# Optimization experiments

Hardware: AMD Instinct MI355X
Metric: run time of the kernel (lower is better)

The kernel has to match this reference:

```python
import jax, jax.numpy as jnp
import numpy as np

B, T, N_X, N_U, N_Y, H = 2048, 2048, 4, 2, 1, 64
MIN_X = jnp.array([0.0, 0.0, 0.0, -jnp.inf], dtype=jnp.float32)
MAX_X = jnp.array([10.0, 10.0, 10.0, jnp.inf], dtype=jnp.float32)
MIN_Y = jnp.array([0.0], dtype=jnp.float32)
MAX_Y = jnp.array([10.0], dtype=jnp.float32)


def setup_inputs() -> dict:
    key = jax.random.key(0)
    ks = jax.random.split(key, 6)
    return {
        "x_0": jax.random.uniform(ks[0], (B, N_X), dtype=jnp.float32) * 5.0,
        "u": jax.random.normal(ks[1], (B, T, N_U), dtype=jnp.float32),
        "theta_f": jnp.array([0.1925, 0.2429, 0.1697, 0.0444, 0.1642], dtype=jnp.float32),
        "theta_h": jnp.zeros((1,), dtype=jnp.float32),
        "tau_u": jnp.ones((1,), dtype=jnp.float32),
        "tau_y": jnp.ones((1,), dtype=jnp.float32),
        "W1": jax.random.normal(ks[2], (N_X + N_U + 5, H), dtype=jnp.float32) / np.sqrt(N_X + N_U + 5),
        "b1": jnp.zeros((H,), dtype=jnp.float32),
        "W2": jax.random.normal(ks[3], (H, N_X), dtype=jnp.float32) * 0.05,
        "Wh": jax.random.normal(ks[4], (N_X, N_Y), dtype=jnp.float32),
    }


def reference(x_0, u, theta_f, theta_h, tau_u, tau_y, W1, b1, W2, Wh):
    Bc = x_0.shape[0]
    tf = jnp.broadcast_to(theta_f[None, :], (Bc, theta_f.shape[0]))
    scale = tau_u[0] / tau_y[0]

    def f(x, ut):
        feat = jnp.concatenate([x, ut, tf], axis=-1)  # (B, n_x+n_u+5)
        return jnp.tanh(feat @ W1 + b1) @ W2 * scale  # (B, n_x)

    def h(x):
        return x @ Wh + theta_h  # (B, n_y)

    y0 = h(x_0)  # unclamped initial output, as in the torch loop

    def step(carry, ut):
        x_step, y_step = carry
        dx = f(x_step, ut)
        x_raw = x_step + dx
        y_new = jnp.clip(h(x_raw), MIN_Y, MAX_Y)  # y computed from pre-clamp state
        x_new = jnp.clip(x_raw, MIN_X, MAX_X)
        return (x_new, y_new), (x_step, y_step)

    u_t = jnp.moveaxis(u, 1, 0)  # (T, B, n_u)
    _, (xs, ys) = jax.lax.scan(step, (x_0, y0), u_t)
    x = jnp.moveaxis(xs, 0, 1)  # (B, T, n_x)
    y = jnp.moveaxis(ys, 0, 1)  # (B, T, n_y)
    return (x, y)
```

## Files before the change

kernel.cpp:

```cpp
#include <hip/hip_runtime.h>

#define B_SZ 2048
#define T_SZ 2048

using f32x16 = float __attribute__((ext_vector_type(16)));
using f32x2  = float __attribute__((ext_vector_type(2)));

template<int CTRL>
__device__ __forceinline__ float dppf(float v) {
  int r = __builtin_amdgcn_update_dpp(0, __builtin_bit_cast(int, v), CTRL, 0xf, 0xf, true);
  return __builtin_bit_cast(float, r);
}

__device__ __forceinline__ f32x2 pkfma(f32x2 a, f32x2 b, f32x2 c) {
  return __builtin_elementwise_fma(a, b, c);
}

__global__ __launch_bounds__(256) void sss_kernel(
    const float* __restrict__ x0p, const float* __restrict__ up,
    const float* __restrict__ tfp, const float* __restrict__ thp,
    const float* __restrict__ tup, const float* __restrict__ typ,
    const float* __restrict__ W1p, const float* __restrict__ b1p,
    const float* __restrict__ W2p, const float* __restrict__ Whp,
    float* __restrict__ outp)
{
  const int lane = threadIdx.x & 63;
  const int wv   = __builtin_amdgcn_readfirstlane((int)(threadIdx.x >> 6));
  const int grp  = lane >> 4;
  const int sl   = lane & 15;
  const int k    = lane & 3;
  const int b    = blockIdx.x * 16 + wv * 4 + grp;

  const float K = 2.8853900817779268f;
  f32x2 w1_01[6], w1_23[6];
#pragma unroll
  for (int r = 0; r < 6; ++r) {
    w1_01[r] = f32x2{W1p[r * 64 + sl]      * K, W1p[r * 64 + sl + 16] * K};
    w1_23[r] = f32x2{W1p[r * 64 + sl + 32] * K, W1p[r * 64 + sl + 48] * K};
  }
  float ccs[4];
#pragma unroll
  for (int i = 0; i < 4; ++i) {
    const int u = sl + 16 * i;
    float t = b1p[u];
#pragma unroll
    for (int q = 0; q < 5; ++q) t = fmaf(tfp[q], W1p[(6 + q) * 64 + u], t);
    ccs[i] = t * K;
  }
  const f32x2 cc01 = f32x2{ccs[0], ccs[1]};
  const f32x2 cc23 = f32x2{ccs[2], ccs[3]};

  const float scale = tup[0] / typ[0];
  f32x2 wAB[4], wCD[4];
#pragma unroll
  for (int i = 0; i < 4; ++i) {
    const float4 w2r = ((const float4*)W2p)[sl + 16 * i];
    float col[4] = {w2r.x * scale, w2r.y * scale, w2r.z * scale, w2r.w * scale};
    wAB[i] = f32x2{col[k], col[k ^ 1]};
    wCD[i] = f32x2{col[k ^ 2], col[k ^ 3]};
  }

  const float whl = Whp[k];
  const float th  = thp[0];

  const float lo = (k == 3) ? -__builtin_inff() : 0.0f;
  const float hi = (k == 3) ?  __builtin_inff() : 10.0f;

  float xlane = x0p[b * 4 + k];
  float x0v = dppf<0x00>(xlane);
  float x1v = dppf<0x55>(xlane);
  float x2v = dppf<0xAA>(xlane);
  float x3v = dppf<0xFF>(xlane);

  float p0 = xlane * whl;
  p0 += dppf<0xB1>(p0);
  p0 += dppf<0x4E>(p0);
  float yv = p0 + th;

  unsigned voff, vinc;
  if (sl < 4) {
    voff = (unsigned)(b * (T_SZ * 4) + sl) * 4u;
    vinc = 16u;
  } else {
    voff = (unsigned)((unsigned)B_SZ * T_SZ * 4u + (unsigned)b * T_SZ) * 4u;
    vinc = (sl == 4) ? 4u : 0u;
  }
  const bool doSt = (sl < 5);
  const bool is4  = (sl == 4);

  const f32x16* up16 = (const f32x16*)(up + (size_t)b * (T_SZ * 2));
  char* outB = (char*)outp;

  f32x16 uch = up16[0];
  const int NC = T_SZ / 8;

  for (int c = 0; c < NC; ++c) {
    const int g = (c + 1 < NC) ? c + 1 : NC - 1;
    const f32x16 unx = up16[g];
#pragma unroll
    for (int jj = 0; jj < 8; ++jj) {
      const float vdata = is4 ? yv : xlane;
      if (doSt) *(float*)(outB + voff) = vdata;
      voff += vinc;

      const float u0 = uch[2 * jj];
      const float u1 = uch[2 * jj + 1];
      const f32x2 u0p = f32x2{u0, u0};
      const f32x2 u1p = f32x2{u1, u1};

      const f32x2 b01 = pkfma(u1p, w1_01[5], pkfma(u0p, w1_01[4], cc01));
      const f32x2 b23 = pkfma(u1p, w1_23[5], pkfma(u0p, w1_23[4], cc23));

      const f32x2 x0pv = f32x2{x0v, x0v};
      const f32x2 x1pv = f32x2{x1v, x1v};
      const f32x2 x2pv = f32x2{x2v, x2v};
      const f32x2 x3pv = f32x2{x3v, x3v};
      const f32x2 mA01 = pkfma(x1pv, w1_01[1], x0pv * w1_01[0]);
      const f32x2 mB01 = pkfma(x3pv, w1_01[3], x2pv * w1_01[2]);
      const f32x2 a01  = (b01 + mA01) + mB01;
      const f32x2 mA23 = pkfma(x1pv, w1_23[1], x0pv * w1_23[0]);
      const f32x2 mB23 = pkfma(x3pv, w1_23[3], x2pv * w1_23[2]);
      const f32x2 a23  = (b23 + mA23) + mB23;

      float h[4];
      {
        const float av[4] = {a01[0], a01[1], a23[0], a23[1]};
#pragma unroll
        for (int i = 0; i < 4; ++i) {
          const float e  = __builtin_amdgcn_exp2f(av[i]);
          const float rr = __builtin_amdgcn_rcpf(e + 1.0f);
          h[i] = fmaf(-2.0f, rr, 1.0f);
        }
      }

      f32x2 qAB = f32x2{h[0], h[0]} * wAB[0];
      qAB = pkfma(f32x2{h[1], h[1]}, wAB[1], qAB);
      qAB = pkfma(f32x2{h[2], h[2]}, wAB[2], qAB);
      qAB = pkfma(f32x2{h[3], h[3]}, wAB[3], qAB);
      f32x2 qCD = f32x2{h[0], h[0]} * wCD[0];
      qCD = pkfma(f32x2{h[1], h[1]}, wCD[1], qCD);
      qCD = pkfma(f32x2{h[2], h[2]}, wCD[2], qCD);
      qCD = pkfma(f32x2{h[3], h[3]}, wCD[3], qCD);

      float v = (qAB[0] + dppf<0xB1>(qAB[1]))
              + (dppf<0x4E>(qCD[0]) + dppf<0x1B>(qCD[1]));
      v += dppf<0x124>(v);
      v += dppf<0x128>(v);

      const float w = xlane + v;
      xlane = __builtin_amdgcn_fmed3f(w, lo, hi);

      float p = w * whl;
      p += dppf<0xB1>(p);
      p += dppf<0x4E>(p);
      yv = __builtin_amdgcn_fmed3f(p + th, 0.0f, 10.0f);

      x0v = dppf<0x00>(xlane);
      x1v = dppf<0x55>(xlane);
      x2v = dppf<0xAA>(xlane);
      x3v = dppf<0xFF>(xlane);
    }
    uch = unx;
  }
}

extern "C" void kernel_launch(void* const* d_in, const int* in_sizes, int n_in,
                              void* d_out, int out_size, void* d_ws, size_t ws_size,
                              hipStream_t stream) {
  (void)in_sizes; (void)n_in; (void)out_size; (void)d_ws; (void)ws_size;
  sss_kernel<<<dim3(B_SZ / 16), dim3(256), 0, stream>>>(
      (const float*)d_in[0], (const float*)d_in[1], (const float*)d_in[2],
      (const float*)d_in[3], (const float*)d_in[4], (const float*)d_in[5],
      (const float*)d_in[6], (const float*)d_in[7], (const float*)d_in[8],
      (const float*)d_in[9], (float*)d_out);
}
```

Before: 359.4 us.

## Keep full state replicated per lane, reduce all outputs with butterfly DPP

```diff
diff --git a/kernel.cpp b/kernel.cpp
--- a/kernel.cpp
+++ b/kernel.cpp
@@ -12,11 +12,19 @@
   return __builtin_bit_cast(float, r);
 }
 
+template<int CTRL>
+__device__ __forceinline__ f32x2 bstage(f32x2 v) {
+  f32x2 s;
+  s[0] = dppf<CTRL>(v[0]);
+  s[1] = dppf<CTRL>(v[1]);
+  return v + s;
+}
+
 __device__ __forceinline__ f32x2 pkfma(f32x2 a, f32x2 b, f32x2 c) {
   return __builtin_elementwise_fma(a, b, c);
 }
 
-__global__ __launch_bounds__(256) void sss_kernel(
+__global__ __launch_bounds__(256, 1) void sss_kernel(
     const float* __restrict__ x0p, const float* __restrict__ up,
     const float* __restrict__ tfp, const float* __restrict__ thp,
     const float* __restrict__ tup, const float* __restrict__ typ,
@@ -28,7 +36,6 @@
   const int wv   = __builtin_amdgcn_readfirstlane((int)(threadIdx.x >> 6));
   const int grp  = lane >> 4;
   const int sl   = lane & 15;
-  const int k    = lane & 3;
   const int b    = blockIdx.x * 16 + wv * 4 + grp;
 
   const float K = 2.8853900817779268f;
@@ -51,31 +58,21 @@
   const f32x2 cc23 = f32x2{ccs[2], ccs[3]};
 
   const float scale = tup[0] / typ[0];
-  f32x2 wAB[4], wCD[4];
+  f32x2 c01[4], c23[4];
 #pragma unroll
   for (int i = 0; i < 4; ++i) {
     const float4 w2r = ((const float4*)W2p)[sl + 16 * i];
-    float col[4] = {w2r.x * scale, w2r.y * scale, w2r.z * scale, w2r.w * scale};
-    wAB[i] = f32x2{col[k], col[k ^ 1]};
-    wCD[i] = f32x2{col[k ^ 2], col[k ^ 3]};
+    c01[i] = f32x2{w2r.x * scale, w2r.y * scale};
+    c23[i] = f32x2{w2r.z * scale, w2r.w * scale};
   }
 
-  const float whl = Whp[k];
+  const float wh0 = Whp[0], wh1 = Whp[1], wh2 = Whp[2], wh3 = Whp[3];
   const float th  = thp[0];
 
-  const float lo = (k == 3) ? -__builtin_inff() : 0.0f;
-  const float hi = (k == 3) ?  __builtin_inff() : 10.0f;
+  f32x2 x01 = f32x2{x0p[b * 4 + 0], x0p[b * 4 + 1]};
+  f32x2 x23 = f32x2{x0p[b * 4 + 2], x0p[b * 4 + 3]};
 
-  float xlane = x0p[b * 4 + k];
-  float x0v = dppf<0x00>(xlane);
-  float x1v = dppf<0x55>(xlane);
-  float x2v = dppf<0xAA>(xlane);
-  float x3v = dppf<0xFF>(xlane);
-
-  float p0 = xlane * whl;
-  p0 += dppf<0xB1>(p0);
-  p0 += dppf<0x4E>(p0);
-  float yv = p0 + th;
+  float yv = fmaf(x01[0], wh0, fmaf(x01[1], wh1, fmaf(x23[0], wh2, fmaf(x23[1], wh3, th))));
 
   unsigned voff, vinc;
   if (sl < 4) {
@@ -87,6 +84,8 @@
   }
   const bool doSt = (sl < 5);
   const bool is4  = (sl == 4);
+  const bool s1   = sl & 1;
+  const bool s2   = sl & 2;
 
   const f32x16* up16 = (const f32x16*)(up + (size_t)b * (T_SZ * 2));
   char* outB = (char*)outp;
@@ -99,7 +98,10 @@
     const f32x16 unx = up16[g];
 #pragma unroll
     for (int jj = 0; jj < 8; ++jj) {
-      const float vdata = is4 ? yv : xlane;
+      const float t0 = s1 ? x01[1] : x01[0];
+      const float t1 = s1 ? x23[1] : x23[0];
+      const float td = s2 ? t1 : t0;
+      const float vdata = is4 ? yv : td;
       if (doSt) *(float*)(outB + voff) = vdata;
       voff += vinc;
 
@@ -111,15 +113,15 @@
       const f32x2 b01 = pkfma(u1p, w1_01[5], pkfma(u0p, w1_01[4], cc01));
       const f32x2 b23 = pkfma(u1p, w1_23[5], pkfma(u0p, w1_23[4], cc23));
 
-      const f32x2 x0pv = f32x2{x0v, x0v};
-      const f32x2 x1pv = f32x2{x1v, x1v};
-      const f32x2 x2pv = f32x2{x2v, x2v};
-      const f32x2 x3pv = f32x2{x3v, x3v};
-      const f32x2 mA01 = pkfma(x1pv, w1_01[1], x0pv * w1_01[0]);
-      const f32x2 mB01 = pkfma(x3pv, w1_01[3], x2pv * w1_01[2]);
+      const f32x2 x0s = f32x2{x01[0], x01[0]};
+      const f32x2 x1s = f32x2{x01[1], x01[1]};
+      const f32x2 x2s = f32x2{x23[0], x23[0]};
+      const f32x2 x3s = f32x2{x23[1], x23[1]};
+      const f32x2 mA01 = pkfma(x1s, w1_01[1], x0s * w1_01[0]);
+      const f32x2 mB01 = pkfma(x3s, w1_01[3], x2s * w1_01[2]);
       const f32x2 a01  = (b01 + mA01) + mB01;
-      const f32x2 mA23 = pkfma(x1pv, w1_23[1], x0pv * w1_23[0]);
-      const f32x2 mB23 = pkfma(x3pv, w1_23[3], x2pv * w1_23[2]);
+      const f32x2 mA23 = pkfma(x1s, w1_23[1], x0s * w1_23[0]);
+      const f32x2 mB23 = pkfma(x3s, w1_23[3], x2s * w1_23[2]);
       const f32x2 a23  = (b23 + mA23) + mB23;
 
       float h[4];
@@ -132,33 +134,28 @@
           h[i] = fmaf(-2.0f, rr, 1.0f);
         }
       }
+      const f32x2 h0s = f32x2{h[0], h[0]};
+      const f32x2 h1s = f32x2{h[1], h[1]};
+      const f32x2 h2s = f32x2{h[2], h[2]};
+      const f32x2 h3s = f32x2{h[3], h[3]};
 
-      f32x2 qAB = f32x2{h[0], h[0]} * wAB[0];
-      qAB = pkfma(f32x2{h[1], h[1]}, wAB[1], qAB);
-      qAB = pkfma(f32x2{h[2], h[2]}, wAB[2], qAB);
-      qAB = pkfma(f32x2{h[3], h[3]}, wAB[3], qAB);
-      f32x2 qCD = f32x2{h[0], h[0]} * wCD[0];
-      qCD = pkfma(f32x2{h[1], h[1]}, wCD[1], qCD);
-      qCD = pkfma(f32x2{h[2], h[2]}, wCD[2], qCD);
-      qCD = pkfma(f32x2{h[3], h[3]}, wCD[3], qCD);
+      f32x2 p01 = pkfma(h1s, c01[1], h0s * c01[0]) + pkfma(h3s, c01[3], h2s * c01[2]);
+      f32x2 p23 = pkfma(h1s, c23[1], h0s * c23[0]) + pkfma(h3s, c23[3], h2s * c23[2]);
 
-      float v = (qAB[0] + dppf<0xB1>(qAB[1]))
-              + (dppf<0x4E>(qCD[0]) + dppf<0x1B>(qCD[1]));
-      v += dppf<0x124>(v);
-      v += dppf<0x128>(v);
+      p01 = bstage<0xB1>(p01);  p23 = bstage<0xB1>(p23);
+      p01 = bstage<0x4E>(p01);  p23 = bstage<0x4E>(p23);
+      p01 = bstage<0x124>(p01); p23 = bstage<0x124>(p23);
+      p01 = bstage<0x128>(p01); p23 = bstage<0x128>(p23);
 
-      const float w = xlane + v;
-      xlane = __builtin_amdgcn_fmed3f(w, lo, hi);
+      const f32x2 w01 = x01 + p01;
+      const f32x2 w23 = x23 + p23;
 
-      float p = w * whl;
-      p += dppf<0xB1>(p);
-      p += dppf<0x4E>(p);
-      yv = __builtin_amdgcn_fmed3f(p + th, 0.0f, 10.0f);
+      const float yy = fmaf(w01[0], wh0, fmaf(w01[1], wh1, fmaf(w23[0], wh2, w23[1] * wh3)));
+      yv = __builtin_amdgcn_fmed3f(yy + th, 0.0f, 10.0f);
 
-      x0v = dppf<0x00>(xlane);
-      x1v = dppf<0x55>(xlane);
-      x2v = dppf<0xAA>(xlane);
-      x3v = dppf<0xFF>(xlane);
+      x01 = f32x2{__builtin_amdgcn_fmed3f(w01[0], 0.0f, 10.0f),
+                  __builtin_amdgcn_fmed3f(w01[1], 0.0f, 10.0f)};
+      x23 = f32x2{__builtin_amdgcn_fmed3f(w23[0], 0.0f, 10.0f), w23[1]};
     }
     uch = unx;
   }
```

After: 432.3 us. +20.3%, slower.

## Interleave two independent batch recurrences per wavefront to hide latency

Applied to the files above, without the earlier changes.

```diff
diff --git a/kernel.cpp b/kernel.cpp
--- a/kernel.cpp
+++ b/kernel.cpp
@@ -16,7 +16,65 @@
   return __builtin_elementwise_fma(a, b, c);
 }
 
-__global__ __launch_bounds__(256) void sss_kernel(
+#define STEP(S) do {                                                          \
+      const float vdata = is4 ? yv##S : xlane##S;                             \
+      if (doSt) *(float*)(outB + voff##S) = vdata;                            \
+      voff##S += vinc;                                                        \
+      const float u0 = uch##S[2 * jj];                                        \
+      const float u1 = uch##S[2 * jj + 1];                                    \
+      const f32x2 u0p = f32x2{u0, u0};                                        \
+      const f32x2 u1p = f32x2{u1, u1};                                        \
+      const f32x2 b01 = pkfma(u1p, w1_01[5], pkfma(u0p, w1_01[4], cc01));     \
+      const f32x2 b23 = pkfma(u1p, w1_23[5], pkfma(u0p, w1_23[4], cc23));     \
+      const f32x2 x0s = f32x2{x0v##S, x0v##S};                                \
+      const f32x2 x1s = f32x2{x1v##S, x1v##S};                                \
+      const f32x2 x2s = f32x2{x2v##S, x2v##S};                                \
+      const f32x2 x3s = f32x2{x3v##S, x3v##S};                                \
+      const f32x2 mA01 = pkfma(x1s, w1_01[1], x0s * w1_01[0]);                \
+      const f32x2 mB01 = pkfma(x3s, w1_01[3], x2s * w1_01[2]);                \
+      const f32x2 a01  = (b01 + mA01) + mB01;                                 \
+      const f32x2 mA23 = pkfma(x1s, w1_23[1], x0s * w1_23[0]);                \
+      const f32x2 mB23 = pkfma(x3s, w1_23[3], x2s * w1_23[2]);                \
+      const f32x2 a23  = (b23 + mA23) + mB23;                                 \
+      float h[4];                                                             \
+      {                                                                       \
+        const float av[4] = {a01[0], a01[1], a23[0], a23[1]};                 \
+        _Pragma("unroll")                                                     \
+        for (int i = 0; i < 4; ++i) {                                         \
+          const float e  = __builtin_amdgcn_exp2f(av[i]);                     \
+          const float rr = __builtin_amdgcn_rcpf(e + 1.0f);                   \
+          h[i] = fmaf(-2.0f, rr, 1.0f);                                       \
+        }                                                                     \
+      }                                                                       \
+      const f32x2 h0s = f32x2{h[0], h[0]};                                    \
+      const f32x2 h1s = f32x2{h[1], h[1]};                                    \
+      const f32x2 h2s = f32x2{h[2], h[2]};                                    \
+      const f32x2 h3s = f32x2{h[3], h[3]};                                    \
+      f32x2 qAB = h0s * wAB[0];                                               \
+      qAB = pkfma(h1s, wAB[1], qAB);                                          \
+      qAB = pkfma(h2s, wAB[2], qAB);                                          \
+      qAB = pkfma(h3s, wAB[3], qAB);                                          \
+      f32x2 qCD = h0s * wCD[0];                                               \
+      qCD = pkfma(h1s, wCD[1], qCD);                                          \
+      qCD = pkfma(h2s, wCD[2], qCD);                                          \
+      qCD = pkfma(h3s, wCD[3], qCD);                                          \
+      float v = (qAB[0] + dppf<0xB1>(qAB[1]))                                 \
+              + (dppf<0x4E>(qCD[0]) + dppf<0x1B>(qCD[1]));                    \
+      v += dppf<0x124>(v);                                                    \
+      v += dppf<0x128>(v);                                                    \
+      const float w = xlane##S + v;                                           \
+      xlane##S = __builtin_amdgcn_fmed3f(w, lo, hi);                          \
+      float p = w * whl;                                                      \
+      p += dppf<0xB1>(p);                                                     \
+      p += dppf<0x4E>(p);                                                     \
+      yv##S = __builtin_amdgcn_fmed3f(p + th, 0.0f, 10.0f);                   \
+      x0v##S = dppf<0x00>(xlane##S);                                          \
+      x1v##S = dppf<0x55>(xlane##S);                                          \
+      x2v##S = dppf<0xAA>(xlane##S);                                          \
+      x3v##S = dppf<0xFF>(xlane##S);                                          \
+    } while (0)
+
+__global__ __launch_bounds__(256, 1) void sss_kernel(
     const float* __restrict__ x0p, const float* __restrict__ up,
     const float* __restrict__ tfp, const float* __restrict__ thp,
     const float* __restrict__ tup, const float* __restrict__ typ,
@@ -29,7 +87,9 @@
   const int grp  = lane >> 4;
   const int sl   = lane & 15;
   const int k    = lane & 3;
-  const int b    = blockIdx.x * 16 + wv * 4 + grp;
+  const int b0   = blockIdx.x * 32 + wv * 8;
+  const int bA   = b0 + grp;
+  const int bB   = b0 + 4 + grp;
 
   const float K = 2.8853900817779268f;
   f32x2 w1_01[6], w1_23[6];
@@ -66,101 +126,58 @@
   const float lo = (k == 3) ? -__builtin_inff() : 0.0f;
   const float hi = (k == 3) ?  __builtin_inff() : 10.0f;
 
-  float xlane = x0p[b * 4 + k];
-  float x0v = dppf<0x00>(xlane);
-  float x1v = dppf<0x55>(xlane);
-  float x2v = dppf<0xAA>(xlane);
-  float x3v = dppf<0xFF>(xlane);
+  float xlaneA = x0p[bA * 4 + k];
+  float x0vA = dppf<0x00>(xlaneA);
+  float x1vA = dppf<0x55>(xlaneA);
+  float x2vA = dppf<0xAA>(xlaneA);
+  float x3vA = dppf<0xFF>(xlaneA);
+  float xlaneB = x0p[bB * 4 + k];
+  float x0vB = dppf<0x00>(xlaneB);
+  float x1vB = dppf<0x55>(xlaneB);
+  float x2vB = dppf<0xAA>(xlaneB);
+  float x3vB = dppf<0xFF>(xlaneB);
 
-  float p0 = xlane * whl;
-  p0 += dppf<0xB1>(p0);
-  p0 += dppf<0x4E>(p0);
-  float yv = p0 + th;
+  float pA = xlaneA * whl;
+  pA += dppf<0xB1>(pA);
+  pA += dppf<0x4E>(pA);
+  float yvA = pA + th;
+  float pB = xlaneB * whl;
+  pB += dppf<0xB1>(pB);
+  pB += dppf<0x4E>(pB);
+  float yvB = pB + th;
 
-  unsigned voff, vinc;
+  unsigned voffA, voffB, vinc;
   if (sl < 4) {
-    voff = (unsigned)(b * (T_SZ * 4) + sl) * 4u;
+    voffA = (unsigned)(bA * (T_SZ * 4) + sl) * 4u;
+    voffB = (unsigned)(bB * (T_SZ * 4) + sl) * 4u;
     vinc = 16u;
   } else {
-    voff = (unsigned)((unsigned)B_SZ * T_SZ * 4u + (unsigned)b * T_SZ) * 4u;
+    voffA = (unsigned)((unsigned)B_SZ * T_SZ * 4u + (unsigned)bA * T_SZ) * 4u;
+    voffB = (unsigned)((unsigned)B_SZ * T_SZ * 4u + (unsigned)bB * T_SZ) * 4u;
     vinc = (sl == 4) ? 4u : 0u;
   }
   const bool doSt = (sl < 5);
   const bool is4  = (sl == 4);
 
-  const f32x16* up16 = (const f32x16*)(up + (size_t)b * (T_SZ * 2));
+  const f32x16* up16A = (const f32x16*)(up + (size_t)bA * (T_SZ * 2));
+  const f32x16* up16B = (const f32x16*)(up + (size_t)bB * (T_SZ * 2));
   char* outB = (char*)outp;
 
-  f32x16 uch = up16[0];
+  f32x16 uchA = up16A[0];
+  f32x16 uchB = up16B[0];
   const int NC = T_SZ / 8;
 
   for (int c = 0; c < NC; ++c) {
     const int g = (c + 1 < NC) ? c + 1 : NC - 1;
-    const f32x16 unx = up16[g];
+    const f32x16 unxA = up16A[g];
+    const f32x16 unxB = up16B[g];
 #pragma unroll
     for (int jj = 0; jj < 8; ++jj) {
-      const float vdata = is4 ? yv : xlane;
-      if (doSt) *(float*)(outB + voff) = vdata;
-      voff += vinc;
-
-      const float u0 = uch[2 * jj];
-      const float u1 = uch[2 * jj + 1];
-      const f32x2 u0p = f32x2{u0, u0};
-      const f32x2 u1p = f32x2{u1, u1};
-
-      const f32x2 b01 = pkfma(u1p, w1_01[5], pkfma(u0p, w1_01[4], cc01));
-      const f32x2 b23 = pkfma(u1p, w1_23[5], pkfma(u0p, w1_23[4], cc23));
-
-      const f32x2 x0pv = f32x2{x0v, x0v};
-      const f32x2 x1pv = f32x2{x1v, x1v};
-      const f32x2 x2pv = f32x2{x2v, x2v};
-      const f32x2 x3pv = f32x2{x3v, x3v};
-      const f32x2 mA01 = pkfma(x1pv, w1_01[1], x0pv * w1_01[0]);
-      const f32x2 mB01 = pkfma(x3pv, w1_01[3], x2pv * w1_01[2]);
-      const f32x2 a01  = (b01 + mA01) + mB01;
-      const f32x2 mA23 = pkfma(x1pv, w1_23[1], x0pv * w1_23[0]);
-      const f32x2 mB23 = pkfma(x3pv, w1_23[3], x2pv * w1_23[2]);
-      const f32x2 a23  = (b23 + mA23) + mB23;
-
-      float h[4];
-      {
-        const float av[4] = {a01[0], a01[1], a23[0], a23[1]};
-#pragma unroll
-        for (int i = 0; i < 4; ++i) {
-          const float e  = __builtin_amdgcn_exp2f(av[i]);
-          const float rr = __builtin_amdgcn_rcpf(e + 1.0f);
-          h[i] = fmaf(-2.0f, rr, 1.0f);
-        }
-      }
-
-      f32x2 qAB = f32x2{h[0], h[0]} * wAB[0];
-      qAB = pkfma(f32x2{h[1], h[1]}, wAB[1], qAB);
-      qAB = pkfma(f32x2{h[2], h[2]}, wAB[2], qAB);
-      qAB = pkfma(f32x2{h[3], h[3]}, wAB[3], qAB);
-      f32x2 qCD = f32x2{h[0], h[0]} * wCD[0];
-      qCD = pkfma(f32x2{h[1], h[1]}, wCD[1], qCD);
-      qCD = pkfma(f32x2{h[2], h[2]}, wCD[2], qCD);
-      qCD = pkfma(f32x2{h[3], h[3]}, wCD[3], qCD);
-
-      float v = (qAB[0] + dppf<0xB1>(qAB[1]))
-              + (dppf<0x4E>(qCD[0]) + dppf<0x1B>(qCD[1]));
-      v += dppf<0x124>(v);
-      v += dppf<0x128>(v);
-
-      const float w = xlane + v;
-      xlane = __builtin_amdgcn_fmed3f(w, lo, hi);
-
-      float p = w * whl;
-      p += dppf<0xB1>(p);
-      p += dppf<0x4E>(p);
-      yv = __builtin_amdgcn_fmed3f(p + th, 0.0f, 10.0f);
-
-      x0v = dppf<0x00>(xlane);
-      x1v = dppf<0x55>(xlane);
-      x2v = dppf<0xAA>(xlane);
-      x3v = dppf<0xFF>(xlane);
+      STEP(A);
+      STEP(B);
     }
-    uch = unx;
+    uchA = unxA;
+    uchB = unxB;
   }
 }
 
@@ -168,7 +185,7 @@
                               void* d_out, int out_size, void* d_ws, size_t ws_size,
                               hipStream_t stream) {
   (void)in_sizes; (void)n_in; (void)out_size; (void)d_ws; (void)ws_size;
-  sss_kernel<<<dim3(B_SZ / 16), dim3(256), 0, stream>>>(
+  sss_kernel<<<dim3(B_SZ / 32), dim3(256), 0, stream>>>(
       (const float*)d_in[0], (const float*)d_in[1], (const float*)d_in[2],
       (const float*)d_in[3], (const float*)d_in[4], (const float*)d_in[5],
       (const float*)d_in[6], (const float*)d_in[7], (const float*)d_in[8],
```

Measured after the change: 643.8 us. 1.79x slower.
